# Kernel optimization log

Measured on AMD Instinct MI355X. Metric: run time of the kernel, lower is better.

The kernel has to match this reference:

```python
import jax, jax.numpy as jnp
import numpy as np

K = 4  # kernel_size

def setup_inputs() -> dict:
    key = jax.random.key(0)
    k1, k2, k3 = jax.random.split(key, 3)
    B, T, C = 4, 4096, 2048
    x = jax.random.normal(k1, (B, T, C), dtype=jnp.float32)
    # depthwise Conv1d weight (C, 1, K) flattened to (C, K); PyTorch default init scale
    bound = 1.0 / np.sqrt(K)
    weight = jax.random.uniform(k2, (C, K), dtype=jnp.float32, minval=-bound, maxval=bound)
    bias = jax.random.uniform(k3, (C,), dtype=jnp.float32, minval=-bound, maxval=bound)
    return {"x": x, "weight": weight, "bias": bias}

def reference(x, weight, bias):
    # Causal depthwise conv on (B,T,C) directly (no transpose needed in jax):
    # y[b,t,c] = sum_k weight[c,k] * x[b, t-(K-1)+k, c] + bias[c]; out = x + y
    B, T, C = x.shape
    xp = jnp.pad(x, ((0, 0), (K - 1, 0), (0, 0)))  # left-pad time axis
    y = bias[None, None, :]
    for k in range(K):  # small fixed kernel taps
        y = y + xp[:, k:k + T, :] * weight[None, None, :, k]
    return x + y
```

## Files before the change

kernel.cpp:

```cpp
#include <hip/hip_runtime.h>

#define B_DIM 4
#define T_DIM 4096
#define C_DIM 2048
#define KK 4
#define TT 16
#define C4 (C_DIM / 4)

typedef float v4f __attribute__((ext_vector_type(4)));

__global__ __launch_bounds__(256) void canonconv_kernel(
    const float* __restrict__ x,
    const float* __restrict__ w,
    const float* __restrict__ bias,
    float* __restrict__ out)
{
    const int idx   = blockIdx.x * blockDim.x + threadIdx.x;
    const int c4    = idx % C4;
    const int tmp   = idx / C4;
    const int ttile = tmp % (T_DIM / TT);
    const int b     = tmp / (T_DIM / TT);
    const int t0    = ttile * TT;
    const int c     = c4 * 4;

    const v4f* wv = (const v4f*)(w + (size_t)c * KK);
    const v4f a0 = wv[0];
    const v4f a1 = wv[1];
    const v4f a2 = wv[2];
    const v4f a3 = wv[3];
    v4f tap0, tap1, tap2, tap3;
    tap0.x = a0.x; tap0.y = a1.x; tap0.z = a2.x; tap0.w = a3.x;
    tap1.x = a0.y; tap1.y = a1.y; tap1.z = a2.y; tap1.w = a3.y;
    tap2.x = a0.z; tap2.y = a1.z; tap2.z = a2.z; tap2.w = a3.z;
    tap3.x = 1.0f + a0.w; tap3.y = 1.0f + a1.w; tap3.z = 1.0f + a2.w; tap3.w = 1.0f + a3.w;
    const v4f bv = *(const v4f*)(bias + c);

    const float* xb = x   + ((size_t)b * T_DIM) * C_DIM + c;
    float*       ob = out + ((size_t)b * T_DIM) * C_DIM + c;

    v4f xm3, xm2, xm1;
    if (t0 == 0) {
        xm3 = (v4f)0.0f;
        xm2 = (v4f)0.0f;
        xm1 = (v4f)0.0f;
    } else {
        xm3 = *(const v4f*)(xb + (size_t)(t0 - 3) * C_DIM);
        xm2 = *(const v4f*)(xb + (size_t)(t0 - 2) * C_DIM);
        xm1 = *(const v4f*)(xb + (size_t)(t0 - 1) * C_DIM);
    }

    #pragma unroll 8
    for (int i = 0; i < TT; ++i) {
        const size_t off = (size_t)(t0 + i) * C_DIM;
        const v4f xc = *(const v4f*)(xb + off);
        v4f r;
        r.x = fmaf(xc.x, tap3.x, fmaf(xm1.x, tap2.x, fmaf(xm2.x, tap1.x, fmaf(xm3.x, tap0.x, bv.x))));
        r.y = fmaf(xc.y, tap3.y, fmaf(xm1.y, tap2.y, fmaf(xm2.y, tap1.y, fmaf(xm3.y, tap0.y, bv.y))));
        r.z = fmaf(xc.z, tap3.z, fmaf(xm1.z, tap2.z, fmaf(xm2.z, tap1.z, fmaf(xm3.z, tap0.z, bv.z))));
        r.w = fmaf(xc.w, tap3.w, fmaf(xm1.w, tap2.w, fmaf(xm2.w, tap1.w, fmaf(xm3.w, tap0.w, bv.w))));
        __builtin_nontemporal_store(r, (v4f*)(ob + off));
        xm3 = xm2;
        xm2 = xm1;
        xm1 = xc;
    }
}

extern "C" void kernel_launch(void* const* d_in, const int* in_sizes, int n_in,
                              void* d_out, int out_size, void* d_ws, size_t ws_size,
                              hipStream_t stream) {
    const float* x    = (const float*)d_in[0];
    const float* w    = (const float*)d_in[1];
    const float* bias = (const float*)d_in[2];
    float* out = (float*)d_out;

    const int total_threads = B_DIM * (T_DIM / TT) * C4;
    const int block = 256;
    const int grid  = total_threads / block;
    canonconv_kernel<<<grid, block, 0, stream>>>(x, w, bias, out);
}
```

Before: 239.9 us.

## Compute one output vector per thread, loading the previous taps from cache

Replaces the per-thread 16-step time loop, which kept a sliding register window, with one thread per (b,t,c4) vector. Each thread loads its own row plus the three previous rows and masks taps at the sequence start. This gives 16x more threads and more memory-level parallelism with no serial loop. The cost is four global loads per output instead of roughly 1.2, with the reuse left to L2 and the infinity cache.

```diff
diff --git a/kernel.cpp b/kernel.cpp
--- a/kernel.cpp
+++ b/kernel.cpp
@@ -4,7 +4,6 @@
 #define T_DIM 4096
 #define C_DIM 2048
 #define KK 4
-#define TT 16
 #define C4 (C_DIM / 4)
 
 typedef float v4f __attribute__((ext_vector_type(4)));
@@ -15,54 +14,53 @@
     const float* __restrict__ bias,
     float* __restrict__ out)
 {
-    const int idx   = blockIdx.x * blockDim.x + threadIdx.x;
-    const int c4    = idx % C4;
-    const int tmp   = idx / C4;
-    const int ttile = tmp % (T_DIM / TT);
-    const int b     = tmp / (T_DIM / TT);
-    const int t0    = ttile * TT;
-    const int c     = c4 * 4;
+    const int i4  = blockIdx.x * blockDim.x + threadIdx.x;
+    const int c4  = i4 & (C4 - 1);
+    const int row = i4 >> 9;
+    const int t   = row & (T_DIM - 1);
+    const int c   = c4 * 4;
+
+    const v4f* xv = (const v4f*)x;
+
+    const int o1 = (t >= 1) ? (i4 - 1 * C4) : i4;
+    const int o2 = (t >= 2) ? (i4 - 2 * C4) : i4;
+    const int o3 = (t >= 3) ? (i4 - 3 * C4) : i4;
+
+    const v4f x0  = xv[i4];
+    const v4f xm1 = xv[o1];
+    const v4f xm2 = xv[o2];
+    const v4f xm3 = xv[o3];
 
     const v4f* wv = (const v4f*)(w + (size_t)c * KK);
-    const v4f a0 = wv[0];
-    const v4f a1 = wv[1];
-    const v4f a2 = wv[2];
-    const v4f a3 = wv[3];
-    v4f tap0, tap1, tap2, tap3;
-    tap0.x = a0.x; tap0.y = a1.x; tap0.z = a2.x; tap0.w = a3.x;
-    tap1.x = a0.y; tap1.y = a1.y; tap1.z = a2.y; tap1.w = a3.y;
-    tap2.x = a0.z; tap2.y = a1.z; tap2.z = a2.z; tap2.w = a3.z;
-    tap3.x = 1.0f + a0.w; tap3.y = 1.0f + a1.w; tap3.z = 1.0f + a2.w; tap3.w = 1.0f + a3.w;
+    v4f a0 = wv[0];
+    v4f a1 = wv[1];
+    v4f a2 = wv[2];
+    v4f a3 = wv[3];
     const v4f bv = *(const v4f*)(bias + c);
 
-    const float* xb = x   + ((size_t)b * T_DIM) * C_DIM + c;
-    float*       ob = out + ((size_t)b * T_DIM) * C_DIM + c;
+    const float m1 = (t >= 1) ? 1.0f : 0.0f;
+    const float m2 = (t >= 2) ? 1.0f : 0.0f;
+    const float m3 = (t >= 3) ? 1.0f : 0.0f;
 
-    v4f xm3, xm2, xm1;
-    if (t0 == 0) {
-        xm3 = (v4f)0.0f;
-        xm2 = (v4f)0.0f;
-        xm1 = (v4f)0.0f;
-    } else {
-        xm3 = *(const v4f*)(xb + (size_t)(t0 - 3) * C_DIM);
-        xm2 = *(const v4f*)(xb + (size_t)(t0 - 2) * C_DIM);
-        xm1 = *(const v4f*)(xb + (size_t)(t0 - 1) * C_DIM);
-    }
+    v4f r;
+    r.x = fmaf(x0.x, 1.0f + a0.w,
+          fmaf(xm1.x, m1 * a0.z,
+          fmaf(xm2.x, m2 * a0.y,
+          fmaf(xm3.x, m3 * a0.x, bv.x))));
+    r.y = fmaf(x0.y, 1.0f + a1.w,
+          fmaf(xm1.y, m1 * a1.z,
+          fmaf(xm2.y, m2 * a1.y,
+          fmaf(xm3.y, m3 * a1.x, bv.y))));
+    r.z = fmaf(x0.z, 1.0f + a2.w,
+          fmaf(xm1.z, m1 * a2.z,
+          fmaf(xm2.z, m2 * a2.y,
+          fmaf(xm3.z, m3 * a2.x, bv.z))));
+    r.w = fmaf(x0.w, 1.0f + a3.w,
+          fmaf(xm1.w, m1 * a3.z,
+          fmaf(xm2.w, m2 * a3.y,
+          fmaf(xm3.w, m3 * a3.x, bv.w))));
 
-    #pragma unroll 8
-    for (int i = 0; i < TT; ++i) {
-        const size_t off = (size_t)(t0 + i) * C_DIM;
-        const v4f xc = *(const v4f*)(xb + off);
-        v4f r;
-        r.x = fmaf(xc.x, tap3.x, fmaf(xm1.x, tap2.x, fmaf(xm2.x, tap1.x, fmaf(xm3.x, tap0.x, bv.x))));
-        r.y = fmaf(xc.y, tap3.y, fmaf(xm1.y, tap2.y, fmaf(xm2.y, tap1.y, fmaf(xm3.y, tap0.y, bv.y))));
-        r.z = fmaf(xc.z, tap3.z, fmaf(xm1.z, tap2.z, fmaf(xm2.z, tap1.z, fmaf(xm3.z, tap0.z, bv.z))));
-        r.w = fmaf(xc.w, tap3.w, fmaf(xm1.w, tap2.w, fmaf(xm2.w, tap1.w, fmaf(xm3.w, tap0.w, bv.w))));
-        __builtin_nontemporal_store(r, (v4f*)(ob + off));
-        xm3 = xm2;
-        xm2 = xm1;
-        xm1 = xc;
-    }
+    __builtin_nontemporal_store(r, ((v4f*)out) + i4);
 }
 
 extern "C" void kernel_launch(void* const* d_in, const int* in_sizes, int n_in,
@@ -73,7 +71,7 @@
     const float* bias = (const float*)d_in[2];
     float* out = (float*)d_out;
 
-    const int total_threads = B_DIM * (T_DIM / TT) * C4;
+    const int total_threads = B_DIM * T_DIM * C4;
     const int block = 256;
     const int grid  = total_threads / block;
     canonconv_kernel<<<grid, block, 0, stream>>>(x, w, bias, out);
```

Result: slower. 278.5 us (+16.1%).
